# Kernel tuning notes

Hardware: AMD Instinct MI355X
Metric: run time of the kernel (lower is better)

## Reference

```python
import jax, jax.numpy as jnp
import numpy as np
import math

B, T, O, D, H, L, FF = 2, 1024, 512, 1024, 16, 4, 4096
MAX_SEQ = 1024


def _ln(x, g, b, eps=1e-5):
    m = jnp.mean(x, -1, keepdims=True)
    v = jnp.mean((x - m) ** 2, -1, keepdims=True)
    return (x - m) * jax.lax.rsqrt(v + eps) * g + b


def _gelu(x):
    return jax.nn.gelu(x, approximate=False)  # torch nn.GELU default = exact erf


def setup_inputs() -> dict:
    key = jax.random.key(0)
    ks = iter(jax.random.split(key, 64))
    std = 0.02
    def w(shape):
        return (jax.random.normal(next(ks), shape, jnp.float32) * std)
    d = {
        'obs': jax.random.normal(next(ks), (B, T, O), jnp.float32),
        # encoder MLP: Linear(O,D), LN, GELU, Linear(D,D), GELU, Linear(D,D), LN
        'enc_w1': w((O, D)), 'enc_b1': jnp.zeros((D,)),
        'enc_g1': jnp.ones((D,)), 'enc_be1': jnp.zeros((D,)),
        'enc_w2': w((D, D)), 'enc_b2': jnp.zeros((D,)),
        'enc_w3': w((D, D)), 'enc_b3': jnp.zeros((D,)),
        'enc_g2': jnp.ones((D,)), 'enc_be2': jnp.zeros((D,)),
        'pos_emb': w((MAX_SEQ, D)),
        # stacked per-layer transformer params [L, ...]
        'ln1_g': jnp.ones((L, D)), 'ln1_b': jnp.zeros((L, D)),
        'wq': w((L, D, D)), 'bq': jnp.zeros((L, D)),
        'wk': w((L, D, D)), 'bk': jnp.zeros((L, D)),
        'wv': w((L, D, D)), 'bv': jnp.zeros((L, D)),
        'wo': w((L, D, D)), 'bo': jnp.zeros((L, D)),
        'ln2_g': jnp.ones((L, D)), 'ln2_b': jnp.zeros((L, D)),
        'mlp_w1': w((L, D, FF)), 'mlp_b1': jnp.zeros((L, FF)),
        'mlp_w2': w((L, FF, D)), 'mlp_b2': jnp.zeros((L, D)),
        'lnf_g': jnp.ones((D,)), 'lnf_b': jnp.zeros((D,)),
        'dec_w': w((D, O)), 'dec_b': jnp.zeros((O,)),
    }
    return d


def reference(obs, enc_w1, enc_b1, enc_g1, enc_be1, enc_w2, enc_b2, enc_w3, enc_b3,
              enc_g2, enc_be2, pos_emb, ln1_g, ln1_b, wq, bq, wk, bk, wv, bv, wo, bo,
              ln2_g, ln2_b, mlp_w1, mlp_b1, mlp_w2, mlp_b2, lnf_g, lnf_b, dec_w, dec_b):
    b, t, _ = obs.shape
    dh = D // H
    scale = 1.0 / math.sqrt(dh)
    # embedder MLP
    h = _gelu(_ln(obs @ enc_w1 + enc_b1, enc_g1, enc_be1))
    h = _gelu(h @ enc_w2 + enc_b2)
    h = _ln(h @ enc_w3 + enc_b3, enc_g2, enc_be2)
    x = h + pos_emb[:t]
    # causal mask [t, t]
    mask = jnp.tril(jnp.ones((t, t), bool))

    def block(x, p):
        g1, b1, Wq, Bq, Wk, Bk, Wv, Bv, Wo, Bo, g2, b2, W1, B1, W2, B2 = p
        hn = _ln(x, g1, b1)
        q = (hn @ Wq + Bq).reshape(b, t, H, dh).transpose(0, 2, 1, 3)
        k = (hn @ Wk + Bk).reshape(b, t, H, dh).transpose(0, 2, 1, 3)
        v = (hn @ Wv + Bv).reshape(b, t, H, dh).transpose(0, 2, 1, 3)
        att = jnp.einsum('bhtd,bhsd->bhts', q, k) * scale
        att = jnp.where(mask, att, -jnp.inf)
        att = jax.nn.softmax(att, axis=-1)
        y = jnp.einsum('bhts,bhsd->bhtd', att, v)
        y = y.transpose(0, 2, 1, 3).reshape(b, t, D)
        x = x + y @ Wo + Bo
        hm = _ln(x, g2, b2)
        x = x + _gelu(hm @ W1 + B1) @ W2 + B2
        return x, None

    stacked = (ln1_g, ln1_b, wq, bq, wk, bk, wv, bv, wo, bo,
               ln2_g, ln2_b, mlp_w1, mlp_b1, mlp_w2, mlp_b2)
    x, _ = jax.lax.scan(block, x, stacked)
    x = _ln(x, lnf_g, lnf_b)
    out_obs = x @ dec_w + dec_b
    return x, out_obs
```

## Files before the change

kernel.cpp:

```cpp
#include <hip/hip_runtime.h>
#include <utility>

typedef unsigned short u16;
typedef __bf16  bf16x8 __attribute__((ext_vector_type(8)));
typedef float   f32x4  __attribute__((ext_vector_type(4)));
typedef unsigned short u16x4 __attribute__((ext_vector_type(4)));

constexpr int Bc = 2, Tc = 1024, Oc = 512, Dc = 1024, Hc = 16, Lc = 4, FFc = 4096;
constexpr int Mc = Bc * Tc;
constexpr int Sq = 3 * Dc;

__device__ __forceinline__ u16 f2b(float f) {
    unsigned u = __float_as_uint(f);
    u = (u + 0x7fffu + ((u >> 16) & 1u)) >> 16;
    return (u16)u;
}
__device__ __forceinline__ float gelu_f(float x) {
    return 0.5f * x * (1.0f + erff(x * 0.7071067811865476f));
}

typedef const __attribute__((address_space(1))) void* gas_p;
typedef __attribute__((address_space(3))) void* las_p;
__device__ __forceinline__ void gload16(const void* g, void* l) {
    __builtin_amdgcn_global_load_lds((gas_p)g, (las_p)l, 16, 0, 0);
}

__global__ __launch_bounds__(256) void wtrans(const float* __restrict__ in,
                                              u16* __restrict__ out, int R, int C,
                                              long inBatch, long outBatch) {
    __shared__ float t[32][33];
    const float* inp = in + (size_t)blockIdx.z * inBatch;
    u16* outp = out + (size_t)blockIdx.z * outBatch;
    const int tx = threadIdx.x & 31, ty = threadIdx.x >> 5;
    const int br = blockIdx.y * 32, bc = blockIdx.x * 32;
#pragma unroll
    for (int i = 0; i < 32; i += 8)
        t[ty + i][tx] = inp[(size_t)(br + ty + i) * C + bc + tx];
    __syncthreads();
#pragma unroll
    for (int i = 0; i < 32; i += 8)
        outp[(size_t)(bc + ty + i) * R + br + tx] = f2b(t[tx][ty + i]);
}

__global__ __launch_bounds__(256) void cvt_bf(const float* __restrict__ in,
                                              u16* __restrict__ out, int n) {
    int i = blockIdx.x * 256 + threadIdx.x;
    if (i * 4 >= n) return;
    float4 v = ((const float4*)in)[i];
    u16x4 r;
    r[0] = f2b(v.x); r[1] = f2b(v.y); r[2] = f2b(v.z); r[3] = f2b(v.w);
    ((u16x4*)out)[i] = r;
}

__global__ __launch_bounds__(256) void pack_qkv_bias(const float* __restrict__ bq,
    const float* __restrict__ bk, const float* __restrict__ bv, float* __restrict__ out) {
    int i = blockIdx.x * 256 + threadIdx.x;
    int l = i / Sq, j = i % Sq;
    float v = (j < Dc) ? bq[l * Dc + j] : (j < 2 * Dc ? bk[l * Dc + j - Dc] : bv[l * Dc + j - 2 * Dc]);
    out[i] = v;
}

__global__ __launch_bounds__(256) void ln_kernel(
    const float* __restrict__ in, const float* __restrict__ gam,
    const float* __restrict__ bet, const float* __restrict__ pos,
    float* __restrict__ outf, u16* __restrict__ outb, int do_gelu) {
    const int row = blockIdx.x, tid = threadIdx.x;
    const float4 v = ((const float4*)(in + (size_t)row * Dc))[tid];
    float s  = v.x + v.y + v.z + v.w;
    float ss = v.x * v.x + v.y * v.y + v.z * v.z + v.w * v.w;
#pragma unroll
    for (int m = 1; m < 64; m <<= 1) {
        s  += __shfl_xor(s,  m, 64);
        ss += __shfl_xor(ss, m, 64);
    }
    __shared__ float red[8];
    const int w = tid >> 6;
    if ((tid & 63) == 0) { red[w] = s; red[4 + w] = ss; }
    __syncthreads();
    s  = red[0] + red[1] + red[2] + red[3];
    ss = red[4] + red[5] + red[6] + red[7];
    const float mean = s * (1.0f / Dc);
    const float rstd = rsqrtf(ss * (1.0f / Dc) - mean * mean + 1e-5f);
    const float4 gv = ((const float4*)gam)[tid];
    const float4 bv = ((const float4*)bet)[tid];
    float y0 = (v.x - mean) * rstd * gv.x + bv.x;
    float y1 = (v.y - mean) * rstd * gv.y + bv.y;
    float y2 = (v.z - mean) * rstd * gv.z + bv.z;
    float y3 = (v.w - mean) * rstd * gv.w + bv.w;
    if (do_gelu) { y0 = gelu_f(y0); y1 = gelu_f(y1); y2 = gelu_f(y2); y3 = gelu_f(y3); }
    if (pos) {
        const float4 pv = ((const float4*)(pos + (size_t)(row & (Tc - 1)) * Dc))[tid];
        y0 += pv.x; y1 += pv.y; y2 += pv.z; y3 += pv.w;
    }
    if (outf) {
        float4 o; o.x = y0; o.y = y1; o.z = y2; o.w = y3;
        ((float4*)(outf + (size_t)row * Dc))[tid] = o;
    }
    if (outb) {
        u16x4 r; r[0] = f2b(y0); r[1] = f2b(y1); r[2] = f2b(y2); r[3] = f2b(y3);
        ((u16x4*)(outb + (size_t)row * Dc))[tid] = r;
    }
}

__global__ __launch_bounds__(256) void red2_ln(
    const float* __restrict__ p, const float* __restrict__ bias,
    const float* __restrict__ resid, float* __restrict__ xfout,
    const float* __restrict__ gam, const float* __restrict__ bet,
    float* __restrict__ lnoutf, u16* __restrict__ lnoutb) {
    const int row = blockIdx.x, tid = threadIdx.x;
    const f32x4 a  = ((const f32x4*)(p + (size_t)row * Dc))[tid];
    const f32x4 b  = ((const f32x4*)(p + (size_t)Mc * Dc + (size_t)row * Dc))[tid];
    const f32x4 bb = ((const f32x4*)bias)[tid];
    const f32x4 r  = ((const f32x4*)(resid + (size_t)row * Dc))[tid];
    f32x4 v;
#pragma unroll
    for (int j = 0; j < 4; ++j) v[j] = a[j] + b[j] + bb[j] + r[j];
    ((f32x4*)(xfout + (size_t)row * Dc))[tid] = v;
    float s  = v[0] + v[1] + v[2] + v[3];
    float ss = v[0]*v[0] + v[1]*v[1] + v[2]*v[2] + v[3]*v[3];
#pragma unroll
    for (int m = 1; m < 64; m <<= 1) {
        s  += __shfl_xor(s,  m, 64);
        ss += __shfl_xor(ss, m, 64);
    }
    __shared__ float red[8];
    const int w = tid >> 6;
    if ((tid & 63) == 0) { red[w] = s; red[4 + w] = ss; }
    __syncthreads();
    s  = red[0] + red[1] + red[2] + red[3];
    ss = red[4] + red[5] + red[6] + red[7];
    const float mean = s * (1.0f / Dc);
    const float rstd = rsqrtf(ss * (1.0f / Dc) - mean * mean + 1e-5f);
    const f32x4 gv = ((const f32x4*)gam)[tid];
    const f32x4 bv = ((const f32x4*)bet)[tid];
    f32x4 y;
#pragma unroll
    for (int j = 0; j < 4; ++j) y[j] = (v[j] - mean) * rstd * gv[j] + bv[j];
    if (lnoutf) ((f32x4*)(lnoutf + (size_t)row * Dc))[tid] = y;
    u16x4 o;
#pragma unroll
    for (int j = 0; j < 4; ++j) o[j] = f2b(y[j]);
    ((u16x4*)(lnoutb + (size_t)row * Dc))[tid] = o;
}

template<int BM, int BN, int FM, int FN, int WM, int WN, int OCC>
__global__ __launch_bounds__(256, OCC) void gemm_k(
    const u16* __restrict__ A, const u16* __restrict__ Bt,
    const float* __restrict__ bias, const float* resid,
    float* Cf, u16* Cb, u16* vTout, int vcol0,
    int M, int N, int Kst, int Kl, int do_gelu) {
    __shared__ u16 sA[2][BM][64];
    __shared__ u16 sB[2][BN][64];
    constexpr int NA = BM / 32;
    constexpr int NB = BN / 32;
    const int tid = threadIdx.x;
    const int lane = tid & 63, w = tid >> 6;
    const int lr = lane & 15, g = lane >> 4;
    const int wm = w / WN, wn = w % WN;

    A  += (size_t)blockIdx.z * Kl;
    Bt += (size_t)blockIdx.z * Kl;
    Cf += (size_t)blockIdx.z * M * N;

    const int gx = gridDim.x;
    const int nwg = gx * gridDim.y;
    const int orig = blockIdx.y * gx + blockIdx.x;
    const int wgid = (orig & 7) * (nwg >> 3) + (orig >> 3);
    const int s = wgid >> 6, q = wgid & 63;
    const int nsx = gx >> 3;
    const int sy = s / nsx, sx = s - sy * nsx;
    const int by = sy * 8 + (q >> 3), bx = sx * 8 + (q & 7);
    const long m0 = (long)by * BM, n0 = (long)bx * BN;

    const f32x4 fzero = {0.f, 0.f, 0.f, 0.f};
    f32x4 acc[FM][FN];
#pragma unroll
    for (int i = 0; i < FM; ++i)
#pragma unroll
        for (int j = 0; j < FN; ++j) acc[i][j] = fzero;

    const int nt = Kl / 64;
    const int srow = lane >> 3, scc = lane & 7;
    const u16* pa[NA];
    const u16* pb[NB];
#pragma unroll
    for (int r = 0; r < NA; ++r)
        pa[r] = A + (size_t)(m0 + r * 32 + w * 8 + srow) * Kst + ((scc ^ srow) * 8);
#pragma unroll
    for (int r = 0; r < NB; ++r)
        pb[r] = Bt + (size_t)(n0 + r * 32 + w * 8 + srow) * Kst + ((scc ^ srow) * 8);

    auto stage = [&](auto curc, int t) {
        constexpr int cu = decltype(curc)::value;
        if (t < nt) {
#pragma unroll
            for (int r = 0; r < NA; ++r) { gload16(pa[r], &sA[cu][r * 32 + w * 8][0]); pa[r] += 64; }
#pragma unroll
            for (int r = 0; r < NB; ++r) { gload16(pb[r], &sB[cu][r * 32 + w * 8][0]); pb[r] += 64; }
        }
    };
    auto compute = [&](auto curc) {
        constexpr int cu = decltype(curc)::value;
#pragma unroll
        for (int ks = 0; ks < 2; ++ks) {
            bf16x8 fa[FM], fb[FN];
#pragma unroll
            for (int mi = 0; mi < FM; ++mi) {
                int row = wm * (16 * FM) + mi * 16 + lr;
                fa[mi] = *(const bf16x8*)&sA[cu][row][((ks * 4 + g) ^ (row & 7)) * 8];
            }
#pragma unroll
            for (int ni = 0; ni < FN; ++ni) {
                int row = wn * (16 * FN) + ni * 16 + lr;
                fb[ni] = *(const bf16x8*)&sB[cu][row][((ks * 4 + g) ^ (row & 7)) * 8];
            }
#pragma unroll
            for (int mi = 0; mi < FM; ++mi)
#pragma unroll
                for (int ni = 0; ni < FN; ++ni)
                    acc[mi][ni] = __builtin_amdgcn_mfma_f32_16x16x32_bf16(
                        fa[mi], fb[ni], acc[mi][ni], 0, 0, 0);
        }
    };
    auto drain_barrier = [&]() {
        asm volatile("s_waitcnt vmcnt(0)" ::: "memory");
        __builtin_amdgcn_sched_barrier(0);
        __syncthreads();
    };

    std::integral_constant<int, 0> c0;
    std::integral_constant<int, 1> c1;
    stage(c0, 0);
    drain_barrier();
    for (int t = 0; t < nt; t += 2) {
        stage(c1, t + 1);
        compute(c0);
        drain_barrier();
        stage(c0, t + 2);
        compute(c1);
        drain_barrier();
    }
#pragma unroll
    for (int mi = 0; mi < FM; ++mi) {
#pragma unroll
        for (int ni = 0; ni < FN; ++ni) {
            const long nc = n0 + wn * (16 * FN) + ni * 16 + lr;
            const float bvv = bias ? bias[nc] : 0.0f;
#pragma unroll
            for (int j = 0; j < 4; ++j) {
                const long mr = m0 + wm * (16 * FM) + mi * 16 + g * 4 + j;
                float v = acc[mi][ni][j] + bvv;
                if (resid) v += resid[(size_t)mr * N + nc];
                if (do_gelu) v = gelu_f(v);
                if (vTout && nc >= vcol0) {
                    const long d = nc - vcol0, t = mr & (Tc - 1), bb = mr >> 10;
                    vTout[((size_t)bb * Dc + d) * Tc + t] = f2b(v);
                } else {
                    if (Cf) Cf[(size_t)mr * N + nc] = v;
                    if (Cb) Cb[(size_t)mr * N + nc] = f2b(v);
                }
            }
        }
    }
}

__global__ __launch_bounds__(256, 2) void attn_kernel(
    const u16* __restrict__ qkv, const u16* __restrict__ Vt, u16* __restrict__ Yg) {
    __shared__ u16 sK[2][64][64];
    __shared__ u16 sV[2][64][64];
    __shared__ u16 sP[4][16][64];
    const int tid = threadIdx.x, w = tid >> 6, lane = tid & 63;
    const int lr = lane & 15, g = lane >> 4;
    const int hw = blockIdx.x;
    const int xcd = hw & 7, slot = hw >> 3;
    const int bh = xcd + 8 * (slot >> 4);
    const int qc = 15 - (slot & 15);
    const int h = bh & 15, b = bh >> 4;
    const int tq0 = qc * 64 + w * 16;
    const u16* Qp = qkv + (size_t)b * Tc * Sq + h * 64;
    const u16* Kp = qkv + (size_t)b * Tc * Sq + Dc + h * 64;
    const u16* Vp = Vt + ((size_t)b * Dc + h * 64) * Tc;

    bf16x8 qf[2];
#pragma unroll
    for (int ks = 0; ks < 2; ++ks)
        qf[ks] = *(const bf16x8*)(Qp + (size_t)(tq0 + lr) * Sq + ks * 32 + g * 8);

    const f32x4 fzero = {0.f, 0.f, 0.f, 0.f};
    f32x4 o[4];
    float mst[4], lst[4];
#pragma unroll
    for (int j = 0; j < 4; ++j) { mst[j] = -1e30f; lst[j] = 0.f; }
#pragma unroll
    for (int ni = 0; ni < 4; ++ni) o[ni] = fzero;

    const int c0 = tid, c1 = tid + 256;
    const int row0 = c0 >> 3, cc0 = c0 & 7;
    const int row1 = c1 >> 3, cc1 = c1 & 7;
    bf16x8 kr[2], vr[2];
    auto kvload = [&](int jk) {
        kr[0] = *(const bf16x8*)(Kp + (size_t)(jk * 64 + row0) * Sq + cc0 * 8);
        kr[1] = *(const bf16x8*)(Kp + (size_t)(jk * 64 + row1) * Sq + cc1 * 8);
        vr[0] = *(const bf16x8*)(Vp + (size_t)row0 * Tc + jk * 64 + cc0 * 8);
        vr[1] = *(const bf16x8*)(Vp + (size_t)row1 * Tc + jk * 64 + cc1 * 8);
    };
    auto kvwrite = [&](int buf) {
        *(bf16x8*)&sK[buf][row0][(cc0 ^ (row0 & 7)) * 8] = kr[0];
        *(bf16x8*)&sK[buf][row1][(cc1 ^ (row1 & 7)) * 8] = kr[1];
        *(bf16x8*)&sV[buf][row0][(cc0 ^ (row0 & 7)) * 8] = vr[0];
        *(bf16x8*)&sV[buf][row1][(cc1 ^ (row1 & 7)) * 8] = vr[1];
    };

    kvload(0);
    kvwrite(0);
    __syncthreads();
    for (int jk = 0; jk <= qc; ++jk) {
        const int cur = jk & 1;
        if (jk < qc) kvload(jk + 1);
        f32x4 s[4];
#pragma unroll
        for (int ni = 0; ni < 4; ++ni) {
            const int row = ni * 16 + lr;
            bf16x8 kf0 = *(const bf16x8*)&sK[cur][row][((0 + g) ^ (lr & 7)) * 8];
            bf16x8 kf1 = *(const bf16x8*)&sK[cur][row][((4 + g) ^ (lr & 7)) * 8];
            s[ni] = __builtin_amdgcn_mfma_f32_16x16x32_bf16(qf[0], kf0, fzero, 0, 0, 0);
            s[ni] = __builtin_amdgcn_mfma_f32_16x16x32_bf16(qf[1], kf1, s[ni], 0, 0, 0);
        }
#pragma unroll
        for (int ni = 0; ni < 4; ++ni)
#pragma unroll
            for (int j = 0; j < 4; ++j) {
                float v = s[ni][j] * 0.125f;
                int tk = jk * 64 + ni * 16 + lr;
                int tq = tq0 + g * 4 + j;
                if (tk > tq) v = -1e30f;
                s[ni][j] = v;
            }
        float fs[4];
#pragma unroll
        for (int j = 0; j < 4; ++j) {
            float pm = fmaxf(fmaxf(s[0][j], s[1][j]), fmaxf(s[2][j], s[3][j]));
            pm = fmaxf(pm, __shfl_xor(pm, 1, 16));
            pm = fmaxf(pm, __shfl_xor(pm, 2, 16));
            pm = fmaxf(pm, __shfl_xor(pm, 4, 16));
            pm = fmaxf(pm, __shfl_xor(pm, 8, 16));
            const float m2 = fmaxf(mst[j], pm);
            fs[j] = __expf(mst[j] - m2);
#pragma unroll
            for (int ni = 0; ni < 4; ++ni)
                s[ni][j] = __expf(s[ni][j] - m2);
            float rsum = s[0][j] + s[1][j] + s[2][j] + s[3][j];
            rsum += __shfl_xor(rsum, 1, 16);
            rsum += __shfl_xor(rsum, 2, 16);
            rsum += __shfl_xor(rsum, 4, 16);
            rsum += __shfl_xor(rsum, 8, 16);
            lst[j] = lst[j] * fs[j] + rsum;
            mst[j] = m2;
        }
#pragma unroll
        for (int ni = 0; ni < 4; ++ni)
#pragma unroll
            for (int j = 0; j < 4; ++j) o[ni][j] *= fs[j];
#pragma unroll
        for (int ni = 0; ni < 4; ++ni)
#pragma unroll
            for (int j = 0; j < 4; ++j) {
                int row = g * 4 + j;
                int col = ni * 16 + lr;
                sP[w][row][(((col >> 3) ^ (row & 7)) << 3) | (col & 7)] = f2b(s[ni][j]);
            }
#pragma unroll
        for (int ks = 0; ks < 2; ++ks) {
            bf16x8 pf = *(const bf16x8*)&sP[w][lr][((ks * 4 + g) ^ (lr & 7)) * 8];
#pragma unroll
            for (int ni = 0; ni < 4; ++ni) {
                const int row = ni * 16 + lr;
                bf16x8 vf = *(const bf16x8*)&sV[cur][row][((ks * 4 + g) ^ (lr & 7)) * 8];
                o[ni] = __builtin_amdgcn_mfma_f32_16x16x32_bf16(pf, vf, o[ni], 0, 0, 0);
            }
        }
        if (jk < qc) kvwrite(cur ^ 1);
        __syncthreads();
    }
#pragma unroll
    for (int ni = 0; ni < 4; ++ni)
#pragma unroll
        for (int j = 0; j < 4; ++j) {
            int tq = tq0 + g * 4 + j;
            int col = h * 64 + ni * 16 + lr;
            Yg[(size_t)(b * Tc + tq) * Dc + col] = f2b(o[ni][j] / lst[j]);
        }
}

extern "C" void kernel_launch(void* const* d_in, const int* in_sizes, int n_in,
                              void* d_out, int out_size, void* d_ws, size_t ws_size,
                              hipStream_t stream) {
    const float* obs    = (const float*)d_in[0];
    const float* enc_w1 = (const float*)d_in[1];
    const float* enc_b1 = (const float*)d_in[2];
    const float* enc_g1 = (const float*)d_in[3];
    const float* enc_be1= (const float*)d_in[4];
    const float* enc_w2 = (const float*)d_in[5];
    const float* enc_b2 = (const float*)d_in[6];
    const float* enc_w3 = (const float*)d_in[7];
    const float* enc_b3 = (const float*)d_in[8];
    const float* enc_g2 = (const float*)d_in[9];
    const float* enc_be2= (const float*)d_in[10];
    const float* pos_emb= (const float*)d_in[11];
    const float* ln1_g  = (const float*)d_in[12];
    const float* ln1_b  = (const float*)d_in[13];
    const float* wq     = (const float*)d_in[14];
    const float* bq     = (const float*)d_in[15];
    const float* wk     = (const float*)d_in[16];
    const float* bk     = (const float*)d_in[17];
    const float* wv     = (const float*)d_in[18];
    const float* bv     = (const float*)d_in[19];
    const float* wo     = (const float*)d_in[20];
    const float* bo     = (const float*)d_in[21];
    const float* ln2_g  = (const float*)d_in[22];
    const float* ln2_b  = (const float*)d_in[23];
    const float* mlp_w1 = (const float*)d_in[24];
    const float* mlp_b1 = (const float*)d_in[25];
    const float* mlp_w2 = (const float*)d_in[26];
    const float* mlp_b2 = (const float*)d_in[27];
    const float* lnf_g  = (const float*)d_in[28];
    const float* lnf_b  = (const float*)d_in[29];
    const float* dec_w  = (const float*)d_in[30];
    const float* dec_b  = (const float*)d_in[31];

    float* out_x = (float*)d_out;
    float* out_o = out_x + (size_t)Mc * Dc;

    char* base = (char*)d_ws;
    size_t off = 0;
    auto ab = [&](size_t e) -> u16* {
        u16* r = (u16*)(base + off); off += (e * 2 + 255) & ~(size_t)255; return r; };
    auto af = [&](size_t e) -> float* {
        float* r = (float*)(base + off); off += (e * 4 + 255) & ~(size_t)255; return r; };

    u16* wt_e1   = ab((size_t)Dc * Oc);
    u16* wt_e2   = ab((size_t)Dc * Dc);
    u16* wt_e3   = ab((size_t)Dc * Dc);
    u16* wtqkv   = ab((size_t)Lc * 3 * Dc * Dc);
    u16* wto     = ab((size_t)Lc * Dc * Dc);
    u16* wtm1    = ab((size_t)Lc * Dc * FFc);
    u16* wtm2    = ab((size_t)Lc * FFc * Dc);
    u16* wt_d    = ab((size_t)Oc * Dc);
    float* qkvb  = af((size_t)Lc * Sq);

    u16*   obs_bf = ab((size_t)Mc * Oc);
    float* tmpf   = af((size_t)Mc * Dc);
    float* xf     = af((size_t)Mc * Dc);
    float* x2f    = af((size_t)Mc * Dc);
    u16*   hn_bf  = ab((size_t)Mc * Dc);
    u16*   qkv    = ab((size_t)Mc * Sq);
    u16*   vT     = ab((size_t)Mc * Dc);
    u16*   y_bf   = ab((size_t)Mc * Dc);
    u16*   ff_bf  = ab((size_t)Mc * FFc);
    float* pk     = af((size_t)2 * Mc * Dc);

    wtrans<<<dim3(Dc / 32, Oc / 32, 1), 256, 0, stream>>>(enc_w1, wt_e1, Oc, Dc, 0, 0);
    wtrans<<<dim3(Dc / 32, Dc / 32, 1), 256, 0, stream>>>(enc_w2, wt_e2, Dc, Dc, 0, 0);
    wtrans<<<dim3(Dc / 32, Dc / 32, 1), 256, 0, stream>>>(enc_w3, wt_e3, Dc, Dc, 0, 0);
    wtrans<<<dim3(Dc / 32, Dc / 32, Lc), 256, 0, stream>>>(wq, wtqkv,            Dc, Dc, (long)Dc * Dc, (long)3 * Dc * Dc);
    wtrans<<<dim3(Dc / 32, Dc / 32, Lc), 256, 0, stream>>>(wk, wtqkv + Dc * Dc,  Dc, Dc, (long)Dc * Dc, (long)3 * Dc * Dc);
    wtrans<<<dim3(Dc / 32, Dc / 32, Lc), 256, 0, stream>>>(wv, wtqkv + 2 * Dc * Dc, Dc, Dc, (long)Dc * Dc, (long)3 * Dc * Dc);
    wtrans<<<dim3(Dc / 32, Dc / 32, Lc), 256, 0, stream>>>(wo, wto, Dc, Dc, (long)Dc * Dc, (long)Dc * Dc);
    wtrans<<<dim3(FFc / 32, Dc / 32, Lc), 256, 0, stream>>>(mlp_w1, wtm1, Dc, FFc, (long)Dc * FFc, (long)Dc * FFc);
    wtrans<<<dim3(Dc / 32, FFc / 32, Lc), 256, 0, stream>>>(mlp_w2, wtm2, FFc, Dc, (long)Dc * FFc, (long)Dc * FFc);
    wtrans<<<dim3(Oc / 32, Dc / 32, 1), 256, 0, stream>>>(dec_w, wt_d, Dc, Oc, 0, 0);
    pack_qkv_bias<<<dim3(Lc * Sq / 256), 256, 0, stream>>>(bq, bk, bv, qkvb);
    cvt_bf<<<dim3((Mc * Oc / 4 + 255) / 256), 256, 0, stream>>>(obs, obs_bf, Mc * Oc);

    auto g128 = [&](const u16* A, const u16* Bt, const float* bias, const float* resid,
                    float* Cf, u16* Cb, u16* vTout, int vcol0,
                    int M, int N, int K, int gel) {
        gemm_k<128, 128, 4, 4, 2, 2, 2><<<dim3(N / 128, M / 128), 256, 0, stream>>>(
            A, Bt, bias, resid, Cf, Cb, vTout, vcol0, M, N, K, K, gel);
    };
    auto g64 = [&](const u16* A, const u16* Bt, const float* bias, const float* resid,
                   float* Cf, u16* Cb, int M, int N, int K, int gel) {
        gemm_k<64, 64, 2, 2, 2, 2, 4><<<dim3(N / 64, M / 64), 256, 0, stream>>>(
            A, Bt, bias, resid, Cf, Cb, nullptr, 0, M, N, K, K, gel);
    };
    auto lnk = [&](const float* in, const float* gg, const float* bb, const float* pos,
                   float* outf, u16* outb, int gel) {
        ln_kernel<<<dim3(Mc), 256, 0, stream>>>(in, gg, bb, pos, outf, outb, gel);
    };

    g64(obs_bf, wt_e1, enc_b1, nullptr, tmpf, nullptr, Mc, Dc, Oc, 0);
    lnk(tmpf, enc_g1, enc_be1, nullptr, nullptr, hn_bf, 1);
    g64(hn_bf, wt_e2, enc_b2, nullptr, nullptr, y_bf, Mc, Dc, Dc, 1);
    g64(y_bf, wt_e3, enc_b3, nullptr, tmpf, nullptr, Mc, Dc, Dc, 0);
    lnk(tmpf, enc_g2, enc_be2, pos_emb, xf, nullptr, 0);

    lnk(xf, ln1_g, ln1_b, nullptr, nullptr, hn_bf, 0);

    for (int l = 0; l < Lc; ++l) {
        g128(hn_bf, wtqkv + (size_t)l * 3 * Dc * Dc, qkvb + (size_t)l * Sq, nullptr,
             nullptr, qkv, vT, 2 * Dc, Mc, Sq, Dc, 0);
        attn_kernel<<<dim3(Bc * Hc * (Tc / 64)), 256, 0, stream>>>(qkv, vT, y_bf);
        g64(y_bf, wto + (size_t)l * Dc * Dc, bo + (size_t)l * Dc, xf, x2f, nullptr, Mc, Dc, Dc, 0);
        lnk(x2f, ln2_g + (size_t)l * Dc, ln2_b + (size_t)l * Dc, nullptr, nullptr, hn_bf, 0);
        g128(hn_bf, wtm1 + (size_t)l * Dc * FFc, mlp_b1 + (size_t)l * FFc, nullptr,
             nullptr, ff_bf, nullptr, 0, Mc, FFc, Dc, 1);
        gemm_k<64, 64, 2, 2, 2, 2, 4><<<dim3(Dc / 64, Mc / 64, 2), 256, 0, stream>>>(
            ff_bf, wtm2 + (size_t)l * FFc * Dc, nullptr, nullptr, pk, nullptr,
            nullptr, 0, Mc, Dc, FFc, FFc / 2, 0);
        if (l < Lc - 1) {
            red2_ln<<<dim3(Mc), 256, 0, stream>>>(
                pk, mlp_b2 + (size_t)l * Dc, x2f, xf,
                ln1_g + (size_t)(l + 1) * Dc, ln1_b + (size_t)(l + 1) * Dc,
                nullptr, hn_bf);
        } else {
            red2_ln<<<dim3(Mc), 256, 0, stream>>>(
                pk, mlp_b2 + (size_t)l * Dc, x2f, xf,
                lnf_g, lnf_b, out_x, hn_bf);
        }
    }

    g64(hn_bf, wt_d, dec_b, nullptr, out_o, nullptr, Mc, Oc, Dc, 0);
}
```

Baseline: 802.5 us.

## Single-buffer GEMMs, retile to 128x64, split-K 4, fuse weight transposes, separate V transpose

Replaces the double-buffered GEMM with a single-buffered variant. QKV and MLP1 now use 128x64 tiles at occupancy 4 instead of 128x128 at occupancy 2, and the MLP2 GEMM splits K four ways with a 4-way reduction in the LN kernel. The ten weight-transpose launches are merged into one table-driven kernel. The V-transpose write is moved out of the GEMM epilogue into a separate bf16 transpose kernel. This trades load/compute overlap for higher occupancy and more blocks, at the cost of extra partial-sum traffic and an extra launch per layer.

```diff
diff --git a/kernel.cpp b/kernel.cpp
--- a/kernel.cpp
+++ b/kernel.cpp
@@ -25,21 +25,54 @@
     __builtin_amdgcn_global_load_lds((gas_p)g, (las_p)l, 16, 0, 0);
 }
 
-__global__ __launch_bounds__(256) void wtrans(const float* __restrict__ in,
-                                              u16* __restrict__ out, int R, int C,
-                                              long inBatch, long outBatch) {
+struct WTSeg {
+    const float* src; u16* dst;
+    int R, C, tilesPerZ;
+    long inB, outB, cumEnd;
+};
+struct WTTab { WTSeg e[10]; };
+
+__global__ __launch_bounds__(256) void uber_wtrans(WTTab tab) {
     __shared__ float t[32][33];
-    const float* inp = in + (size_t)blockIdx.z * inBatch;
-    u16* outp = out + (size_t)blockIdx.z * outBatch;
+    const long id = blockIdx.x;
+    int s = 0;
+#pragma unroll
+    for (int i = 0; i < 10; ++i)
+        if (id >= tab.e[i].cumEnd) s = i + 1;
+    const WTSeg e = tab.e[s];
+    const long start = (s == 0) ? 0 : tab.e[s - 1].cumEnd;
+    const long local = id - start;
+    const int z = (int)(local / e.tilesPerZ);
+    const long tt = local % e.tilesPerZ;
+    const int ntx = e.C >> 5;
+    const int txb = (int)(tt % ntx), tyb = (int)(tt / ntx);
+    const float* inp = e.src + (size_t)z * e.inB;
+    u16* outp = e.dst + (size_t)z * e.outB;
+    const int tx = threadIdx.x & 31, ty = threadIdx.x >> 5;
+    const int br = tyb * 32, bc = txb * 32;
+#pragma unroll
+    for (int i = 0; i < 32; i += 8)
+        t[ty + i][tx] = inp[(size_t)(br + ty + i) * e.C + bc + tx];
+    __syncthreads();
+#pragma unroll
+    for (int i = 0; i < 32; i += 8)
+        outp[(size_t)(bc + ty + i) * e.R + br + tx] = f2b(t[tx][ty + i]);
+}
+
+__global__ __launch_bounds__(256) void btrans(const u16* __restrict__ in,
+                                              u16* __restrict__ out, int inStride) {
+    __shared__ u16 t[32][33];
+    const u16* inp = in + (size_t)blockIdx.z * Tc * inStride;
+    u16* outp = out + (size_t)blockIdx.z * Dc * Tc;
     const int tx = threadIdx.x & 31, ty = threadIdx.x >> 5;
     const int br = blockIdx.y * 32, bc = blockIdx.x * 32;
 #pragma unroll
     for (int i = 0; i < 32; i += 8)
-        t[ty + i][tx] = inp[(size_t)(br + ty + i) * C + bc + tx];
+        t[ty + i][tx] = inp[(size_t)(br + ty + i) * inStride + bc + tx];
     __syncthreads();
 #pragma unroll
     for (int i = 0; i < 32; i += 8)
-        outp[(size_t)(bc + ty + i) * R + br + tx] = f2b(t[tx][ty + i]);
+        outp[(size_t)(bc + ty + i) * Tc + br + tx] = t[tx][ty + i];
 }
 
 __global__ __launch_bounds__(256) void cvt_bf(const float* __restrict__ in,
@@ -102,19 +135,24 @@
     }
 }
 
+template<int NP>
 __global__ __launch_bounds__(256) void red2_ln(
     const float* __restrict__ p, const float* __restrict__ bias,
     const float* __restrict__ resid, float* __restrict__ xfout,
     const float* __restrict__ gam, const float* __restrict__ bet,
     float* __restrict__ lnoutf, u16* __restrict__ lnoutb) {
     const int row = blockIdx.x, tid = threadIdx.x;
-    const f32x4 a  = ((const f32x4*)(p + (size_t)row * Dc))[tid];
-    const f32x4 b  = ((const f32x4*)(p + (size_t)Mc * Dc + (size_t)row * Dc))[tid];
     const f32x4 bb = ((const f32x4*)bias)[tid];
     const f32x4 r  = ((const f32x4*)(resid + (size_t)row * Dc))[tid];
     f32x4 v;
 #pragma unroll
-    for (int j = 0; j < 4; ++j) v[j] = a[j] + b[j] + bb[j] + r[j];
+    for (int j = 0; j < 4; ++j) v[j] = bb[j] + r[j];
+#pragma unroll
+    for (int pl = 0; pl < NP; ++pl) {
+        const f32x4 a = ((const f32x4*)(p + (size_t)pl * Mc * Dc + (size_t)row * Dc))[tid];
+#pragma unroll
+        for (int j = 0; j < 4; ++j) v[j] += a[j];
+    }
     ((f32x4*)(xfout + (size_t)row * Dc))[tid] = v;
     float s  = v[0] + v[1] + v[2] + v[3];
     float ss = v[0]*v[0] + v[1]*v[1] + v[2]*v[2] + v[3]*v[3];
@@ -143,25 +181,7 @@
     ((u16x4*)(lnoutb + (size_t)row * Dc))[tid] = o;
 }
 
-template<int BM, int BN, int FM, int FN, int WM, int WN, int OCC>
-__global__ __launch_bounds__(256, OCC) void gemm_k(
-    const u16* __restrict__ A, const u16* __restrict__ Bt,
-    const float* __restrict__ bias, const float* resid,
-    float* Cf, u16* Cb, u16* vTout, int vcol0,
-    int M, int N, int Kst, int Kl, int do_gelu) {
-    __shared__ u16 sA[2][BM][64];
-    __shared__ u16 sB[2][BN][64];
-    constexpr int NA = BM / 32;
-    constexpr int NB = BN / 32;
-    const int tid = threadIdx.x;
-    const int lane = tid & 63, w = tid >> 6;
-    const int lr = lane & 15, g = lane >> 4;
-    const int wm = w / WN, wn = w % WN;
-
-    A  += (size_t)blockIdx.z * Kl;
-    Bt += (size_t)blockIdx.z * Kl;
-    Cf += (size_t)blockIdx.z * M * N;
-
+__device__ __forceinline__ void xcd_map(int& bx, int& by) {
     const int gx = gridDim.x;
     const int nwg = gx * gridDim.y;
     const int orig = blockIdx.y * gx + blockIdx.x;
@@ -169,7 +189,30 @@
     const int s = wgid >> 6, q = wgid & 63;
     const int nsx = gx >> 3;
     const int sy = s / nsx, sx = s - sy * nsx;
-    const int by = sy * 8 + (q >> 3), bx = sx * 8 + (q & 7);
+    by = sy * 8 + (q >> 3);
+    bx = sx * 8 + (q & 7);
+}
+
+template<int BM, int BN, int FM, int FN, int WM, int WN, int OCC>
+__global__ __launch_bounds__(256, OCC) void gemm_s(
+    const u16* __restrict__ A, const u16* __restrict__ Bt,
+    const float* __restrict__ bias, const float* resid,
+    float* Cf, u16* Cb, int M, int N, int Kst, int Kl, int do_gelu) {
+    __shared__ u16 sA[BM][64];
+    __shared__ u16 sB[BN][64];
+    constexpr int NA = BM / 32;
+    constexpr int NB = BN / 32;
+    const int tid = threadIdx.x;
+    const int lane = tid & 63, w = tid >> 6;
+    const int lr = lane & 15, g = lane >> 4;
+    const int wm = w / WN, wn = w % WN;
+
+    A  += (size_t)blockIdx.z * Kl;
+    Bt += (size_t)blockIdx.z * Kl;
+    Cf += (size_t)blockIdx.z * M * N;
+
+    int bx, by;
+    xcd_map(bx, by);
     const long m0 = (long)by * BM, n0 = (long)bx * BN;
 
     const f32x4 fzero = {0.f, 0.f, 0.f, 0.f};
@@ -190,29 +233,26 @@
     for (int r = 0; r < NB; ++r)
         pb[r] = Bt + (size_t)(n0 + r * 32 + w * 8 + srow) * Kst + ((scc ^ srow) * 8);
 
-    auto stage = [&](auto curc, int t) {
-        constexpr int cu = decltype(curc)::value;
-        if (t < nt) {
-#pragma unroll
-            for (int r = 0; r < NA; ++r) { gload16(pa[r], &sA[cu][r * 32 + w * 8][0]); pa[r] += 64; }
-#pragma unroll
-            for (int r = 0; r < NB; ++r) { gload16(pb[r], &sB[cu][r * 32 + w * 8][0]); pb[r] += 64; }
-        }
-    };
-    auto compute = [&](auto curc) {
-        constexpr int cu = decltype(curc)::value;
+    for (int t = 0; t < nt; ++t) {
+#pragma unroll
+        for (int r = 0; r < NA; ++r) { gload16(pa[r], &sA[r * 32 + w * 8][0]); pa[r] += 64; }
+#pragma unroll
+        for (int r = 0; r < NB; ++r) { gload16(pb[r], &sB[r * 32 + w * 8][0]); pb[r] += 64; }
+        asm volatile("s_waitcnt vmcnt(0)" ::: "memory");
+        __builtin_amdgcn_sched_barrier(0);
+        __syncthreads();
 #pragma unroll
         for (int ks = 0; ks < 2; ++ks) {
             bf16x8 fa[FM], fb[FN];
 #pragma unroll
             for (int mi = 0; mi < FM; ++mi) {
                 int row = wm * (16 * FM) + mi * 16 + lr;
-                fa[mi] = *(const bf16x8*)&sA[cu][row][((ks * 4 + g) ^ (row & 7)) * 8];
+                fa[mi] = *(const bf16x8*)&sA[row][((ks * 4 + g) ^ (row & 7)) * 8];
             }
 #pragma unroll
             for (int ni = 0; ni < FN; ++ni) {
                 int row = wn * (16 * FN) + ni * 16 + lr;
-                fb[ni] = *(const bf16x8*)&sB[cu][row][((ks * 4 + g) ^ (row & 7)) * 8];
+                fb[ni] = *(const bf16x8*)&sB[row][((ks * 4 + g) ^ (row & 7)) * 8];
             }
 #pragma unroll
             for (int mi = 0; mi < FM; ++mi)
@@ -221,24 +261,7 @@
                     acc[mi][ni] = __builtin_amdgcn_mfma_f32_16x16x32_bf16(
                         fa[mi], fb[ni], acc[mi][ni], 0, 0, 0);
         }
-    };
-    auto drain_barrier = [&]() {
-        asm volatile("s_waitcnt vmcnt(0)" ::: "memory");
-        __builtin_amdgcn_sched_barrier(0);
         __syncthreads();
-    };
-
-    std::integral_constant<int, 0> c0;
-    std::integral_constant<int, 1> c1;
-    stage(c0, 0);
-    drain_barrier();
-    for (int t = 0; t < nt; t += 2) {
-        stage(c1, t + 1);
-        compute(c0);
-        drain_barrier();
-        stage(c0, t + 2);
-        compute(c1);
-        drain_barrier();
     }
 #pragma unroll
     for (int mi = 0; mi < FM; ++mi) {
@@ -252,13 +275,8 @@
                 float v = acc[mi][ni][j] + bvv;
                 if (resid) v += resid[(size_t)mr * N + nc];
                 if (do_gelu) v = gelu_f(v);
-                if (vTout && nc >= vcol0) {
-                    const long d = nc - vcol0, t = mr & (Tc - 1), bb = mr >> 10;
-                    vTout[((size_t)bb * Dc + d) * Tc + t] = f2b(v);
-                } else {
-                    if (Cf) Cf[(size_t)mr * N + nc] = v;
-                    if (Cb) Cb[(size_t)mr * N + nc] = f2b(v);
-                }
+                if (Cf) Cf[(size_t)mr * N + nc] = v;
+                if (Cb) Cb[(size_t)mr * N + nc] = f2b(v);
             }
         }
     }
@@ -457,31 +475,39 @@
     u16*   vT     = ab((size_t)Mc * Dc);
     u16*   y_bf   = ab((size_t)Mc * Dc);
     u16*   ff_bf  = ab((size_t)Mc * FFc);
-    float* pk     = af((size_t)2 * Mc * Dc);
-
-    wtrans<<<dim3(Dc / 32, Oc / 32, 1), 256, 0, stream>>>(enc_w1, wt_e1, Oc, Dc, 0, 0);
-    wtrans<<<dim3(Dc / 32, Dc / 32, 1), 256, 0, stream>>>(enc_w2, wt_e2, Dc, Dc, 0, 0);
-    wtrans<<<dim3(Dc / 32, Dc / 32, 1), 256, 0, stream>>>(enc_w3, wt_e3, Dc, Dc, 0, 0);
-    wtrans<<<dim3(Dc / 32, Dc / 32, Lc), 256, 0, stream>>>(wq, wtqkv,            Dc, Dc, (long)Dc * Dc, (long)3 * Dc * Dc);
-    wtrans<<<dim3(Dc / 32, Dc / 32, Lc), 256, 0, stream>>>(wk, wtqkv + Dc * Dc,  Dc, Dc, (long)Dc * Dc, (long)3 * Dc * Dc);
-    wtrans<<<dim3(Dc / 32, Dc / 32, Lc), 256, 0, stream>>>(wv, wtqkv + 2 * Dc * Dc, Dc, Dc, (long)Dc * Dc, (long)3 * Dc * Dc);
-    wtrans<<<dim3(Dc / 32, Dc / 32, Lc), 256, 0, stream>>>(wo, wto, Dc, Dc, (long)Dc * Dc, (long)Dc * Dc);
-    wtrans<<<dim3(FFc / 32, Dc / 32, Lc), 256, 0, stream>>>(mlp_w1, wtm1, Dc, FFc, (long)Dc * FFc, (long)Dc * FFc);
-    wtrans<<<dim3(Dc / 32, FFc / 32, Lc), 256, 0, stream>>>(mlp_w2, wtm2, FFc, Dc, (long)Dc * FFc, (long)Dc * FFc);
-    wtrans<<<dim3(Oc / 32, Dc / 32, 1), 256, 0, stream>>>(dec_w, wt_d, Dc, Oc, 0, 0);
+    float* pk     = af((size_t)4 * Mc * Dc);
+
+    WTTab tab;
+    long cum = 0;
+    auto seg = [&](int i, const float* src, u16* dst, int R, int C, int nz,
+                   long inB, long outB) {
+        int tpz = (R / 32) * (C / 32);
+        cum += (long)tpz * nz;
+        tab.e[i] = WTSeg{src, dst, R, C, tpz, inB, outB, cum};
+    };
+    seg(0, enc_w1, wt_e1, Oc, Dc, 1, 0, 0);
+    seg(1, enc_w2, wt_e2, Dc, Dc, 1, 0, 0);
+    seg(2, enc_w3, wt_e3, Dc, Dc, 1, 0, 0);
+    seg(3, wq, wtqkv,              Dc, Dc, Lc, (long)Dc * Dc, (long)3 * Dc * Dc);
+    seg(4, wk, wtqkv + Dc * Dc,    Dc, Dc, Lc, (long)Dc * Dc, (long)3 * Dc * Dc);
+    seg(5, wv, wtqkv + 2 * Dc * Dc,Dc, Dc, Lc, (long)Dc * Dc, (long)3 * Dc * Dc);
+    seg(6, wo, wto, Dc, Dc, Lc, (long)Dc * Dc, (long)Dc * Dc);
+    seg(7, mlp_w1, wtm1, Dc, FFc, Lc, (long)Dc * FFc, (long)Dc * FFc);
+    seg(8, mlp_w2, wtm2, FFc, Dc, Lc, (long)Dc * FFc, (long)Dc * FFc);
+    seg(9, dec_w, wt_d, Dc, Oc, 1, 0, 0);
+    uber_wtrans<<<dim3((unsigned)cum), 256, 0, stream>>>(tab);
     pack_qkv_bias<<<dim3(Lc * Sq / 256), 256, 0, stream>>>(bq, bk, bv, qkvb);
     cvt_bf<<<dim3((Mc * Oc / 4 + 255) / 256), 256, 0, stream>>>(obs, obs_bf, Mc * Oc);
 
-    auto g128 = [&](const u16* A, const u16* Bt, const float* bias, const float* resid,
-                    float* Cf, u16* Cb, u16* vTout, int vcol0,
-                    int M, int N, int K, int gel) {
-        gemm_k<128, 128, 4, 4, 2, 2, 2><<<dim3(N / 128, M / 128), 256, 0, stream>>>(
-            A, Bt, bias, resid, Cf, Cb, vTout, vcol0, M, N, K, K, gel);
+    auto gS = [&](const u16* A, const u16* Bt, const float* bias, const float* resid,
+                  float* Cf, u16* Cb, int M, int N, int K, int gel) {
+        gemm_s<128, 64, 4, 2, 2, 2, 4><<<dim3(N / 64, M / 128), 256, 0, stream>>>(
+            A, Bt, bias, resid, Cf, Cb, M, N, K, K, gel);
     };
     auto g64 = [&](const u16* A, const u16* Bt, const float* bias, const float* resid,
                    float* Cf, u16* Cb, int M, int N, int K, int gel) {
-        gemm_k<64, 64, 2, 2, 2, 2, 4><<<dim3(N / 64, M / 64), 256, 0, stream>>>(
-            A, Bt, bias, resid, Cf, Cb, nullptr, 0, M, N, K, K, gel);
+        gemm_s<64, 64, 2, 2, 2, 2, 4><<<dim3(N / 64, M / 64), 256, 0, stream>>>(
+            A, Bt, bias, resid, Cf, Cb, M, N, K, K, gel);
     };
     auto lnk = [&](const float* in, const float* gg, const float* bb, const float* pos,
                    float* outf, u16* outb, int gel) {
@@ -497,23 +523,24 @@
     lnk(xf, ln1_g, ln1_b, nullptr, nullptr, hn_bf, 0);
 
     for (int l = 0; l < Lc; ++l) {
-        g128(hn_bf, wtqkv + (size_t)l * 3 * Dc * Dc, qkvb + (size_t)l * Sq, nullptr,
-             nullptr, qkv, vT, 2 * Dc, Mc, Sq, Dc, 0);
+        gS(hn_bf, wtqkv + (size_t)l * 3 * Dc * Dc, qkvb + (size_t)l * Sq, nullptr,
+           nullptr, qkv, Mc, Sq, Dc, 0);
+        btrans<<<dim3(Dc / 32, Tc / 32, Bc), 256, 0, stream>>>(qkv + 2 * Dc, vT, Sq);
         attn_kernel<<<dim3(Bc * Hc * (Tc / 64)), 256, 0, stream>>>(qkv, vT, y_bf);
         g64(y_bf, wto + (size_t)l * Dc * Dc, bo + (size_t)l * Dc, xf, x2f, nullptr, Mc, Dc, Dc, 0);
         lnk(x2f, ln2_g + (size_t)l * Dc, ln2_b + (size_t)l * Dc, nullptr, nullptr, hn_bf, 0);
-        g128(hn_bf, wtm1 + (size_t)l * Dc * FFc, mlp_b1 + (size_t)l * FFc, nullptr,
-             nullptr, ff_bf, nullptr, 0, Mc, FFc, Dc, 1);
-        gemm_k<64, 64, 2, 2, 2, 2, 4><<<dim3(Dc / 64, Mc / 64, 2), 256, 0, stream>>>(
+        gS(hn_bf, wtm1 + (size_t)l * Dc * FFc, mlp_b1 + (size_t)l * FFc, nullptr,
+           nullptr, ff_bf, Mc, FFc, Dc, 1);
+        gemm_s<128, 64, 4, 2, 2, 2, 4><<<dim3(Dc / 64, Mc / 128, 4), 256, 0, stream>>>(
             ff_bf, wtm2 + (size_t)l * FFc * Dc, nullptr, nullptr, pk, nullptr,
-            nullptr, 0, Mc, Dc, FFc, FFc / 2, 0);
+            Mc, Dc, FFc, FFc / 4, 0);
         if (l < Lc - 1) {
-            red2_ln<<<dim3(Mc), 256, 0, stream>>>(
+            red2_ln<4><<<dim3(Mc), 256, 0, stream>>>(
                 pk, mlp_b2 + (size_t)l * Dc, x2f, xf,
                 ln1_g + (size_t)(l + 1) * Dc, ln1_b + (size_t)(l + 1) * Dc,
                 nullptr, hn_bf);
         } else {
-            red2_ln<<<dim3(Mc), 256, 0, stream>>>(
+            red2_ln<4><<<dim3(Mc), 256, 0, stream>>>(
                 pk, mlp_b2 + (size_t)l * Dc, x2f, xf,
                 lnf_g, lnf_b, out_x, hn_bf);
         }
```

Result: faster. 733.0 us (-8.7%).
